# Kernel optimization log

Hardware: AMD Instinct MI355X
Metric: run time of the kernel (lower is better)

Reference implementation:

```python
import jax, jax.numpy as jnp
import numpy as np

EPS_LN1 = 1e-6   # partial(nn.LayerNorm, eps=1e-6)
EPS_OUT = 1e-5   # nn.LayerNorm default inside SS3D out_norm


def _layernorm(x, w, b, eps):
    m = jnp.mean(x, axis=-1, keepdims=True)
    v = jnp.var(x, axis=-1, keepdims=True)
    return (x - m) * jax.lax.rsqrt(v + eps) * w + b


def _selective_scan(dA, dBx):
    # dA, dBx: (B, K, d, L, N); linear recurrence h_t = dA_t * h_{t-1} + dBx_t
    def comb(c1, c2):
        a1, b1 = c1
        a2, b2 = c2
        return a2 * a1, a2 * b1 + b2
    _, hs = jax.lax.associative_scan(comb, (dA, dBx), axis=3)
    return hs  # (B, K, d, L, N)


def setup_inputs() -> dict:
    key = jax.random.key(0)
    ks = jax.random.split(key, 12)
    B, D, H, W, C = 1, 16, 16, 16, 96
    d, N, K, R = 96, 16, 6, 6  # d_inner, d_state, n_scan_dirs, dt_rank
    s = 0.02
    f = lambda k, shp: jax.random.normal(k, shp, dtype=jnp.float32)
    return {
        "x": f(ks[0], (B, D, H, W, C)),
        "ln1_w": jnp.ones((C,), jnp.float32),
        "ln1_b": jnp.zeros((C,), jnp.float32),
        "in_proj_w": f(ks[1], (2 * d, C)) * s,
        "conv_w": f(ks[2], (d, 1, 3, 3, 3)) * s,
        "conv_b": f(ks[3], (d,)) * s,
        "x_proj_w": f(ks[4], (K, R + 2 * N, d)) * s,
        "dt_proj_w": f(ks[5], (K, d, R)) * s,
        "dt_proj_b": f(ks[6], (K, d)) * s,
        "A_log": jnp.log(1.0 + 15.0 * jax.random.uniform(ks[7], (K, d, N), jnp.float32)),
        "D_skip": f(ks[8], (K, d)) * s,
        "out_norm_w": jnp.ones((d,), jnp.float32),
        "out_norm_b": jnp.zeros((d,), jnp.float32),
        "out_proj_w": f(ks[9], (C, d)) * s,
    }


def reference(x, ln1_w, ln1_b, in_proj_w, conv_w, conv_b, x_proj_w,
              dt_proj_w, dt_proj_b, A_log, D_skip, out_norm_w, out_norm_b,
              out_proj_w):
    B, D, H, W, C = x.shape
    L = D * H * W
    K, _, d = x_proj_w.shape
    R = dt_proj_w.shape[2]
    N = A_log.shape[2]

    # pre-norm
    xn = _layernorm(x, ln1_w, ln1_b, EPS_LN1)

    # in_proj -> (x, z)
    xz = jnp.einsum('bdhwc,ec->bdhwe', xn, in_proj_w)  # (B,D,H,W,2d)
    xh, z = jnp.split(xz, 2, axis=-1)

    # depthwise 3x3x3 conv + SiLU, channels-first
    xc = jnp.transpose(xh, (0, 4, 1, 2, 3))  # (B,d,D,H,W)
    xc = jax.lax.conv_general_dilated(
        xc, conv_w, window_strides=(1, 1, 1), padding='SAME',
        dimension_numbers=('NCDHW', 'OIDHW', 'NCDHW'),
        feature_group_count=d)
    xc = jax.nn.silu(xc + conv_b[None, :, None, None, None])

    # K = 6 scan orderings: DHW, HWD, WDH and their reverses
    o0 = xc.reshape(B, d, L)
    o1 = jnp.transpose(xc, (0, 1, 3, 4, 2)).reshape(B, d, L)  # (H,W,D) order
    o2 = jnp.transpose(xc, (0, 1, 4, 2, 3)).reshape(B, d, L)  # (W,D,H) order
    fwd3 = jnp.stack([o0, o1, o2], axis=1)                    # (B,3,d,L)
    xs = jnp.concatenate([fwd3, jnp.flip(fwd3, axis=-1)], axis=1)  # (B,K,d,L)

    # per-direction input-dependent parameters
    x_dbl = jnp.einsum('bkdl,kcd->bkcl', xs, x_proj_w)        # (B,K,R+2N,L)
    dt, Bm, Cm = jnp.split(x_dbl, [R, R + N], axis=2)
    dts = jnp.einsum('bkrl,kdr->bkdl', dt, dt_proj_w) + dt_proj_b[None, :, :, None]
    dts = jax.nn.softplus(dts)                                # delta_softplus

    A = -jnp.exp(A_log)                                       # (K,d,N)
    dA = jnp.exp(dts[..., None] * A[None, :, :, None, :])     # (B,K,d,L,N)
    Bt = jnp.transpose(Bm, (0, 1, 3, 2))                      # (B,K,L,N)
    dBx = (dts * xs)[..., None] * Bt[:, :, None, :, :]        # (B,K,d,L,N)

    hs = _selective_scan(dA, dBx)                             # (B,K,d,L,N)
    Ct = jnp.transpose(Cm, (0, 1, 3, 2))                      # (B,K,L,N)
    ys = jnp.einsum('bkdln,bkln->bkdl', hs, Ct) + D_skip[None, :, :, None] * xs

    # undo reversals and orderings, sum the 6 paths
    yf = ys[:, :3] + jnp.flip(ys[:, 3:], axis=-1)             # (B,3,d,L)
    y0 = yf[:, 0]
    y1 = jnp.transpose(yf[:, 1].reshape(B, d, H, W, D), (0, 1, 4, 2, 3)).reshape(B, d, L)
    y2 = jnp.transpose(yf[:, 2].reshape(B, d, W, D, H), (0, 1, 3, 4, 2)).reshape(B, d, L)
    y = (y0 + y1 + y2).reshape(B, d, D, H, W)
    y = jnp.transpose(y, (0, 2, 3, 4, 1))                     # (B,D,H,W,d)

    # out_norm, gate, out_proj
    y = _layernorm(y, out_norm_w, out_norm_b, EPS_OUT)
    y = y * jax.nn.silu(z)
    out = jnp.einsum('bdhwe,ce->bdhwc', y, out_proj_w)

    # residual (drop_path is identity at eval)
    return x + out
```

## Files before the change

### kernel.cpp

```cpp
#include <hip/hip_runtime.h>
#include <hip/hip_bf16.h>

#define L 4096
#define CDIM 96
#define DDIM 96
#define KDIR 6
#define NST 16
#define RRK 6
#define YH 32
#define NCHUNK 256
#define CHLEN 16

typedef _Float16 half4v __attribute__((ext_vector_type(4)));

__device__ __forceinline__ float sigmoidf_(float x) { return 1.f / (1.f + __expf(-x)); }

__device__ __forceinline__ int sigma_k(int kb, int l) {
    if (kb == 0) return l;
    if (kb == 1) return ((l & 15) << 8) | ((l >> 8) << 4) | ((l >> 4) & 15);
    return (((l >> 4) & 15) << 8) | ((l & 15) << 4) | (l >> 8);
}

__global__ void __launch_bounds__(192) k1_ln_inproj(
        const float* __restrict__ x, const float* __restrict__ ln_w,
        const float* __restrict__ ln_b, const float* __restrict__ Wp,
        _Float16* __restrict__ xhh, _Float16* __restrict__ zsh) {
    int s0 = blockIdx.x * 8;
    int tid = threadIdx.x;
    __shared__ __align__(16) float xt[8][96];
    __shared__ __align__(16) float xn[8][96];
    __shared__ float mss[8], rss[8];
    ((float4*)&xt[0][0])[tid] = ((const float4*)(x + (size_t)s0 * 96))[tid];
    __syncthreads();
    int wave = tid >> 6, lane = tid & 63;
    for (int r = wave; r < 8; r += 3) {
        float v = xt[r][lane] + ((lane < 32) ? xt[r][64 + lane] : 0.f);
#pragma unroll
        for (int off = 1; off < 64; off <<= 1) v += __shfl_xor(v, off);
        float vs = xt[r][lane] * xt[r][lane] + ((lane < 32) ? xt[r][64 + lane] * xt[r][64 + lane] : 0.f);
#pragma unroll
        for (int off = 1; off < 64; off <<= 1) vs += __shfl_xor(vs, off);
        if (lane == 0) {
            float mean = v * (1.f / 96.f);
            float var = vs * (1.f / 96.f) - mean * mean;
            mss[r] = mean; rss[r] = rsqrtf(var + 1e-6f);
        }
    }
    __syncthreads();
    {
        int r = tid / 24, c4 = tid % 24;
        float4 xv = ((float4*)&xt[r][0])[c4];
        float4 wv = ((const float4*)ln_w)[c4];
        float4 bv = ((const float4*)ln_b)[c4];
        float m = mss[r], rs = rss[r];
        float4 o;
        o.x = (xv.x - m) * rs * wv.x + bv.x;
        o.y = (xv.y - m) * rs * wv.y + bv.y;
        o.z = (xv.z - m) * rs * wv.z + bv.z;
        o.w = (xv.w - m) * rs * wv.w + bv.w;
        ((float4*)&xn[r][0])[c4] = o;
    }
    float4 Wr[24];
    const float4* wr = (const float4*)(Wp + (size_t)tid * 96);
#pragma unroll
    for (int c4 = 0; c4 < 24; c4++) Wr[c4] = wr[c4];
    __syncthreads();
#pragma unroll
    for (int s = 0; s < 8; s++) {
        const float4* xr4 = (const float4*)&xn[s][0];
        float a0 = 0.f, a1 = 0.f, a2 = 0.f, a3 = 0.f;
#pragma unroll
        for (int c4 = 0; c4 < 24; c4 += 4) {
            float4 x0 = xr4[c4], x1 = xr4[c4 + 1], x2 = xr4[c4 + 2], x3 = xr4[c4 + 3];
            a0 += Wr[c4].x * x0.x + Wr[c4].y * x0.y + Wr[c4].z * x0.z + Wr[c4].w * x0.w;
            a1 += Wr[c4+1].x * x1.x + Wr[c4+1].y * x1.y + Wr[c4+1].z * x1.z + Wr[c4+1].w * x1.w;
            a2 += Wr[c4+2].x * x2.x + Wr[c4+2].y * x2.y + Wr[c4+2].z * x2.z + Wr[c4+2].w * x2.w;
            a3 += Wr[c4+3].x * x3.x + Wr[c4+3].y * x3.y + Wr[c4+3].z * x3.z + Wr[c4+3].w * x3.w;
        }
        float acc = (a0 + a1) + (a2 + a3);
        if (tid < 96) xhh[(size_t)tid * L + s0 + s] = (_Float16)acc;
        else zsh[(size_t)(s0 + s) * 96 + (tid - 96)] = (_Float16)(acc * sigmoidf_(acc));
    }
}

__global__ void k2_conv(const _Float16* __restrict__ xhh, const float* __restrict__ cw,
                        const float* __restrict__ cb, _Float16* __restrict__ xch,
                        _Float16* __restrict__ xcTh) {
    int idx = blockIdx.x * 256 + threadIdx.x;
    int c = idx >> 12, s = idx & 4095;
    int dz = s >> 8, h = (s >> 4) & 15, w = s & 15;
    const _Float16* xin = xhh + (size_t)c * L;
    const float* wc = cw + c * 27;
    float acc = cb[c];
#pragma unroll
    for (int i = 0; i < 3; i++) {
        int z2 = dz + i - 1; if ((unsigned)z2 > 15u) continue;
#pragma unroll
        for (int j = 0; j < 3; j++) {
            int h2 = h + j - 1; if ((unsigned)h2 > 15u) continue;
#pragma unroll
            for (int kk = 0; kk < 3; kk++) {
                int w2 = w + kk - 1; if ((unsigned)w2 > 15u) continue;
                acc += (float)xin[z2 * 256 + h2 * 16 + w2] * wc[i * 9 + j * 3 + kk];
            }
        }
    }
    float r = acc * sigmoidf_(acc);
    _Float16 hr = (_Float16)r;
    xch[(size_t)c * L + s] = hr;
    xcTh[(size_t)s * 96 + c] = hr;
}

__global__ void k3_xproj(const _Float16* __restrict__ xch, const float* __restrict__ Wx,
                         const float* __restrict__ Wdt, const float* __restrict__ bdt,
                         _Float16* __restrict__ Y2h, _Float16* __restrict__ Zsh) {
    int k = blockIdx.x;
    int tid = threadIdx.x;
    int sbase = blockIdx.y * 256;
    int s = sbase + tid;
    int g = blockIdx.z;
    __shared__ float dts[256][6];
    float acc[14];
#pragma unroll
    for (int i = 0; i < 14; i++) acc[i] = 0.f;
    const float* wdt_rows = Wx + (size_t)k * 38 * DDIM;
    const float* wbc      = Wx + ((size_t)k * 38 + 6 + g * 8) * DDIM;
    for (int dd = 0; dd < 96; dd += 4) {
        float v[4];
#pragma unroll
        for (int j = 0; j < 4; j++) v[j] = (float)xch[(size_t)(dd + j) * L + s];
#pragma unroll
        for (int j = 0; j < 4; j++) {
#pragma unroll
            for (int r = 0; r < 6; r++) acc[r] += wdt_rows[r * DDIM + dd + j] * v[j];
#pragma unroll
            for (int i = 0; i < 8; i++) acc[6 + i] += wbc[i * DDIM + dd + j] * v[j];
        }
    }
    _Float16* yo = Y2h + ((size_t)k * L + s) * YH;
#pragma unroll
    for (int i = 0; i < 8; i++) yo[g * 8 + i] = (_Float16)acc[6 + i];
#pragma unroll
    for (int r = 0; r < 6; r++) dts[tid][r] = acc[r];
    __syncthreads();
    for (int i = 0; i < 24; i++) {
        int idx = i * 256 + tid;
        int dl = idx % 24;
        int sr = idx / 24;
        int d = g * 24 + dl;
        const float* wr = Wdt + ((size_t)k * 96 + d) * 6;
        float a = bdt[k * 96 + d];
#pragma unroll
        for (int r = 0; r < 6; r++) a += wr[r] * dts[sr][r];
        float sp = (a > 15.f) ? a : __logf(1.f + __expf(a));
        Zsh[((size_t)k * L + sbase + sr) * 96 + d] = (_Float16)sp;
    }
}


__global__ void __launch_bounds__(256) ka_scan(
        const _Float16* __restrict__ Zsh, const _Float16* __restrict__ xcTh,
        const _Float16* __restrict__ Y2h, const float* __restrict__ A_log,
        _Float16* __restrict__ Aah, _Float16* __restrict__ Abh) {
    int t = blockIdx.x * 256 + threadIdx.x;
    int nq = t & 3;
    int q = t >> 2;
    int d = q % 96;
    int rest = q / 96;
    int chunk = rest % NCHUNK;
    int k = rest / NCHUNK;
    int kb = (k < 3) ? k : (k - 3);
    bool flip = (k >= 3);
    float An[4];
    {
        float4 al = *(const float4*)(A_log + ((size_t)k * 96 + d) * 16 + nq * 4);
        An[0] = -__expf(al.x); An[1] = -__expf(al.y);
        An[2] = -__expf(al.z); An[3] = -__expf(al.w);
    }
    float a[4] = {1.f, 1.f, 1.f, 1.f};
    float b[4] = {0.f, 0.f, 0.f, 0.f};
    const _Float16* Zk = Zsh + (size_t)k * L * 96;
    const _Float16* Yk = Y2h + (size_t)k * L * YH;
    int l0 = chunk * CHLEN;
    for (int i = 0; i < CHLEN; i += 4) {
        int sI[4]; float dt[4], xv[4]; half4v Bh[4];
#pragma unroll
        for (int j = 0; j < 4; j++) {
            int l = l0 + i + j;
            int lp = flip ? (4095 - l) : l;
            sI[j] = sigma_k(kb, lp);
        }
#pragma unroll
        for (int j = 0; j < 4; j++) {
            dt[j] = (float)Zk[(size_t)sI[j] * 96 + d];
            xv[j] = (float)xcTh[(size_t)sI[j] * 96 + d];
            Bh[j] = *(const half4v*)(Yk + (size_t)sI[j] * YH + nq * 4);
        }
#pragma unroll
        for (int j = 0; j < 4; j++) {
            float dtx = dt[j] * xv[j];
            float e0 = __expf(dt[j] * An[0]);
            float e1 = __expf(dt[j] * An[1]);
            float e2 = __expf(dt[j] * An[2]);
            float e3 = __expf(dt[j] * An[3]);
            b[0] = e0 * b[0] + dtx * (float)Bh[j].x; a[0] *= e0;
            b[1] = e1 * b[1] + dtx * (float)Bh[j].y; a[1] *= e1;
            b[2] = e2 * b[2] + dtx * (float)Bh[j].z; a[2] *= e2;
            b[3] = e3 * b[3] + dtx * (float)Bh[j].w; a[3] *= e3;
        }
    }
    size_t o = (((size_t)k * NCHUNK + chunk) * 96 + d) * 16 + nq * 4;
    half4v ha, hb;
    ha.x = (_Float16)a[0]; ha.y = (_Float16)a[1]; ha.z = (_Float16)a[2]; ha.w = (_Float16)a[3];
    hb.x = (_Float16)b[0]; hb.y = (_Float16)b[1]; hb.z = (_Float16)b[2]; hb.w = (_Float16)b[3];
    *(half4v*)(Aah + o) = ha;
    *(half4v*)(Abh + o) = hb;
}

__global__ void __launch_bounds__(256) kb_combine(
        const _Float16* __restrict__ Aah, const _Float16* __restrict__ Abh,
        _Float16* __restrict__ Pbh) {
    int t = blockIdx.x * 256 + threadIdx.x;
    int n = t & 15;
    int rest = t >> 4;
    int d = rest % 96;
    int k = rest / 96;
    size_t base = ((size_t)k * NCHUNK * 96 + d) * 16 + n;
    const size_t cstride = 96 * 16;
    float rb = 0.f;
    for (int c0 = 0; c0 < NCHUNK; c0 += 16) {
        float av[16], bv[16];
#pragma unroll
        for (int j = 0; j < 16; j++) {
            av[j] = (float)Aah[base + (size_t)(c0 + j) * cstride];
            bv[j] = (float)Abh[base + (size_t)(c0 + j) * cstride];
        }
#pragma unroll
        for (int j = 0; j < 16; j++) {
            Pbh[base + (size_t)(c0 + j) * cstride] = (_Float16)rb;
            rb = av[j] * rb + bv[j];
        }
    }
}

__global__ void __launch_bounds__(256) kc_apply(
        const _Float16* __restrict__ Zsh, const _Float16* __restrict__ xcTh,
        const _Float16* __restrict__ Y2h, const float* __restrict__ A_log,
        const float* __restrict__ D_skip, const _Float16* __restrict__ Pbh,
        _Float16* __restrict__ ysh) {
    int t = blockIdx.x * 256 + threadIdx.x;
    int nq = t & 3;
    int q = t >> 2;
    int d = q % 96;
    int rest = q / 96;
    int chunk = rest % NCHUNK;
    int k = rest / NCHUNK;
    int kb = (k < 3) ? k : (k - 3);
    bool flip = (k >= 3);
    float An[4];
    {
        float4 al = *(const float4*)(A_log + ((size_t)k * 96 + d) * 16 + nq * 4);
        An[0] = -__expf(al.x); An[1] = -__expf(al.y);
        An[2] = -__expf(al.z); An[3] = -__expf(al.w);
    }
    float Dk = D_skip[k * DDIM + d];
    float h[4];
    {
        half4v hp = *(const half4v*)(Pbh + (((size_t)k * NCHUNK + chunk) * 96 + d) * 16 + nq * 4);
        h[0] = (float)hp.x; h[1] = (float)hp.y; h[2] = (float)hp.z; h[3] = (float)hp.w;
    }
    const _Float16* Zk = Zsh + (size_t)k * L * 96;
    const _Float16* Yk = Y2h + (size_t)k * L * YH;
    int l0 = chunk * CHLEN;
    for (int i = 0; i < CHLEN; i += 4) {
        int sI[4]; float dt[4], xv[4]; half4v Bh[4], Ch[4];
#pragma unroll
        for (int j = 0; j < 4; j++) {
            int l = l0 + i + j;
            int lp = flip ? (4095 - l) : l;
            sI[j] = sigma_k(kb, lp);
        }
#pragma unroll
        for (int j = 0; j < 4; j++) {
            dt[j] = (float)Zk[(size_t)sI[j] * 96 + d];
            xv[j] = (float)xcTh[(size_t)sI[j] * 96 + d];
            Bh[j] = *(const half4v*)(Yk + (size_t)sI[j] * YH + nq * 4);
            Ch[j] = *(const half4v*)(Yk + (size_t)sI[j] * YH + 16 + nq * 4);
        }
#pragma unroll
        for (int j = 0; j < 4; j++) {
            float dtx = dt[j] * xv[j];
            float e0 = __expf(dt[j] * An[0]);
            float e1 = __expf(dt[j] * An[1]);
            float e2 = __expf(dt[j] * An[2]);
            float e3 = __expf(dt[j] * An[3]);
            h[0] = e0 * h[0] + dtx * (float)Bh[j].x;
            h[1] = e1 * h[1] + dtx * (float)Bh[j].y;
            h[2] = e2 * h[2] + dtx * (float)Bh[j].z;
            h[3] = e3 * h[3] + dtx * (float)Bh[j].w;
            float p = h[0] * (float)Ch[j].x + h[1] * (float)Ch[j].y
                    + h[2] * (float)Ch[j].z + h[3] * (float)Ch[j].w;
            p += __shfl_xor(p, 1);
            p += __shfl_xor(p, 2);
            if (nq == 0) ysh[((size_t)sI[j] * KDIR + k) * 96 + d] = (_Float16)(p + Dk * xv[j]);
        }
    }
}

__global__ void __launch_bounds__(192) k6_out(
        const _Float16* __restrict__ ysh, const _Float16* __restrict__ zsh,
        const float* __restrict__ onw, const float* __restrict__ onb,
        const float* __restrict__ Wo, const float* __restrict__ x,
        float* __restrict__ out) {
    int s0 = blockIdx.x * 8;
    int tid = threadIdx.x;
    __shared__ __align__(16) float vt[8][96];
    __shared__ __align__(16) float gt[8][96];
    __shared__ float mss[8], rss[8];
#pragma unroll
    for (int j = 0; j < 4; j++) {
        int f = tid + j * 192;
        int sr = f / 96, c = f % 96;
        const _Float16* yr = ysh + ((size_t)(s0 + sr) * KDIR) * 96 + c;
        float v = 0.f;
#pragma unroll
        for (int k = 0; k < KDIR; k++) v += (float)yr[k * 96];
        vt[sr][c] = v;
    }
    __syncthreads();
    int wave = tid >> 6, lane = tid & 63;
    for (int r = wave; r < 8; r += 3) {
        float v = vt[r][lane] + ((lane < 32) ? vt[r][64 + lane] : 0.f);
#pragma unroll
        for (int off = 1; off < 64; off <<= 1) v += __shfl_xor(v, off);
        float vs = vt[r][lane] * vt[r][lane] + ((lane < 32) ? vt[r][64 + lane] * vt[r][64 + lane] : 0.f);
#pragma unroll
        for (int off = 1; off < 64; off <<= 1) vs += __shfl_xor(vs, off);
        if (lane == 0) {
            float mean = v * (1.f / 96.f);
            float var = vs * (1.f / 96.f) - mean * mean;
            mss[r] = mean; rss[r] = rsqrtf(var + 1e-5f);
        }
    }
    __syncthreads();
#pragma unroll
    for (int j = 0; j < 4; j++) {
        int f = tid + j * 192;
        int sr = f / 96, c = f % 96;
        float g = (vt[sr][c] - mss[sr]) * rss[sr] * onw[c] + onb[c];
        gt[sr][c] = g * (float)zsh[(size_t)(s0 + sr) * 96 + c];
    }
    int e = tid % 96, sg = tid / 96;
    float4 Wr[24];
    const float4* wr = (const float4*)(Wo + (size_t)e * 96);
#pragma unroll
    for (int c4 = 0; c4 < 24; c4++) Wr[c4] = wr[c4];
    __syncthreads();
#pragma unroll
    for (int j = 0; j < 4; j++) {
        int s = sg * 4 + j;
        const float4* g4 = (const float4*)&gt[s][0];
        float a0 = 0.f, a1 = 0.f, a2 = 0.f, a3 = 0.f;
#pragma unroll
        for (int c4 = 0; c4 < 24; c4 += 4) {
            float4 x0 = g4[c4], x1 = g4[c4 + 1], x2 = g4[c4 + 2], x3 = g4[c4 + 3];
            a0 += Wr[c4].x * x0.x + Wr[c4].y * x0.y + Wr[c4].z * x0.z + Wr[c4].w * x0.w;
            a1 += Wr[c4+1].x * x1.x + Wr[c4+1].y * x1.y + Wr[c4+1].z * x1.z + Wr[c4+1].w * x1.w;
            a2 += Wr[c4+2].x * x2.x + Wr[c4+2].y * x2.y + Wr[c4+2].z * x2.z + Wr[c4+2].w * x2.w;
            a3 += Wr[c4+3].x * x3.x + Wr[c4+3].y * x3.y + Wr[c4+3].z * x3.z + Wr[c4+3].w * x3.w;
        }
        float acc = (a0 + a1) + (a2 + a3) + x[(size_t)(s0 + s) * 96 + e];
        out[(size_t)(s0 + s) * 96 + e] = acc;
    }
}

extern "C" void kernel_launch(void* const* d_in, const int* in_sizes, int n_in,
                              void* d_out, int out_size, void* d_ws, size_t ws_size,
                              hipStream_t stream) {
    const float* x        = (const float*)d_in[0];
    const float* ln1_w    = (const float*)d_in[1];
    const float* ln1_b    = (const float*)d_in[2];
    const float* in_proj  = (const float*)d_in[3];
    const float* conv_w   = (const float*)d_in[4];
    const float* conv_b   = (const float*)d_in[5];
    const float* x_proj   = (const float*)d_in[6];
    const float* dt_w     = (const float*)d_in[7];
    const float* dt_b     = (const float*)d_in[8];
    const float* A_log    = (const float*)d_in[9];
    const float* D_skip   = (const float*)d_in[10];
    const float* onw      = (const float*)d_in[11];
    const float* onb      = (const float*)d_in[12];
    const float* out_w    = (const float*)d_in[13];
    float* out = (float*)d_out;

    _Float16* xhh  = (_Float16*)d_ws;
    _Float16* zsh  = xhh + (size_t)96 * L;
    _Float16* xch  = zsh + (size_t)96 * L;
    _Float16* xcTh = xch + (size_t)96 * L;
    _Float16* Y2h  = xcTh + (size_t)96 * L;
    _Float16* Zsh  = Y2h + (size_t)KDIR * L * YH;
    _Float16* ysh  = Zsh + (size_t)KDIR * L * 96;
    _Float16* Aah  = ysh + (size_t)L * KDIR * 96;
    _Float16* Abh  = Aah + (size_t)KDIR * NCHUNK * DDIM * NST;
    _Float16* Pbh  = Abh + (size_t)KDIR * NCHUNK * DDIM * NST;

    k1_ln_inproj<<<dim3(L / 8), dim3(192), 0, stream>>>(x, ln1_w, ln1_b, in_proj, xhh, zsh);
    k2_conv<<<dim3(96 * L / 256), dim3(256), 0, stream>>>(xhh, conv_w, conv_b, xch, xcTh);
    k3_xproj<<<dim3(KDIR, 16, 4), dim3(256), 0, stream>>>(xch, x_proj, dt_w, dt_b, Y2h, Zsh);
    ka_scan<<<dim3(KDIR * NCHUNK * DDIM * 4 / 256), dim3(256), 0, stream>>>(Zsh, xcTh, Y2h, A_log, Aah, Abh);
    kb_combine<<<dim3(KDIR * DDIM * NST / 256), dim3(256), 0, stream>>>(Aah, Abh, Pbh);
    kc_apply<<<dim3(KDIR * NCHUNK * DDIM * 4 / 256), dim3(256), 0, stream>>>(Zsh, xcTh, Y2h, A_log, D_skip, Pbh, ysh);
    k6_out<<<dim3(L / 8), dim3(192), 0, stream>>>(ysh, zsh, onw, onb, out_w, x, out);
}
```

Baseline: 179.8 us.

## Parallelize chunk-carry combine with wave-level scan and transpose carry layouts

The chunk-carry combine used to run as a serial loop over 256 chunks per (k,d,n) column with only 9216 threads. It now assigns one 64-lane wave per column: each lane folds 4 chunks, then a shuffle-based Hillis-Steele scan computes the prefix carries. To give that wave contiguous reads, the Aah/Abh/Pbh buffers are stored column-major over chunks, which turns the ka_scan stores and kc_apply loads into strided scalar accesses. The ys buffer is also reordered to put the 6 directions innermost, so k6_out can sum them with three half2 loads while kc_apply's writes become strided.

```diff
diff --git a/kernel.cpp b/kernel.cpp
--- a/kernel.cpp
+++ b/kernel.cpp
@@ -12,6 +12,7 @@
 #define CHLEN 16
 
 typedef _Float16 half4v __attribute__((ext_vector_type(4)));
+typedef _Float16 half2v __attribute__((ext_vector_type(2)));
 
 __device__ __forceinline__ float sigmoidf_(float x) { return 1.f / (1.f + __expf(-x)); }
 
@@ -209,38 +210,41 @@
             b[3] = e3 * b[3] + dtx * (float)Bh[j].w; a[3] *= e3;
         }
     }
-    size_t o = (((size_t)k * NCHUNK + chunk) * 96 + d) * 16 + nq * 4;
-    half4v ha, hb;
-    ha.x = (_Float16)a[0]; ha.y = (_Float16)a[1]; ha.z = (_Float16)a[2]; ha.w = (_Float16)a[3];
-    hb.x = (_Float16)b[0]; hb.y = (_Float16)b[1]; hb.z = (_Float16)b[2]; hb.w = (_Float16)b[3];
-    *(half4v*)(Aah + o) = ha;
-    *(half4v*)(Abh + o) = hb;
+    size_t colbase = ((size_t)(k * 96 + d) * 16 + nq * 4) * NCHUNK + chunk;
+#pragma unroll
+    for (int j = 0; j < 4; j++) {
+        Aah[colbase + (size_t)j * NCHUNK] = (_Float16)a[j];
+        Abh[colbase + (size_t)j * NCHUNK] = (_Float16)b[j];
+    }
 }
 
 __global__ void __launch_bounds__(256) kb_combine(
         const _Float16* __restrict__ Aah, const _Float16* __restrict__ Abh,
         _Float16* __restrict__ Pbh) {
-    int t = blockIdx.x * 256 + threadIdx.x;
-    int n = t & 15;
-    int rest = t >> 4;
-    int d = rest % 96;
-    int k = rest / 96;
-    size_t base = ((size_t)k * NCHUNK * 96 + d) * 16 + n;
-    const size_t cstride = 96 * 16;
-    float rb = 0.f;
-    for (int c0 = 0; c0 < NCHUNK; c0 += 16) {
-        float av[16], bv[16];
-#pragma unroll
-        for (int j = 0; j < 16; j++) {
-            av[j] = (float)Aah[base + (size_t)(c0 + j) * cstride];
-            bv[j] = (float)Abh[base + (size_t)(c0 + j) * cstride];
-        }
-#pragma unroll
-        for (int j = 0; j < 16; j++) {
-            Pbh[base + (size_t)(c0 + j) * cstride] = (_Float16)rb;
-            rb = av[j] * rb + bv[j];
-        }
-    }
+    int w = blockIdx.x * 4 + (threadIdx.x >> 6);
+    int lane = threadIdx.x & 63;
+    size_t colbase = (size_t)w * NCHUNK;
+    half4v ha = *(const half4v*)(Aah + colbase + lane * 4);
+    half4v hb = *(const half4v*)(Abh + colbase + lane * 4);
+    float a0 = (float)ha.x, a1 = (float)ha.y, a2 = (float)ha.z, a3 = (float)ha.w;
+    float b0 = (float)hb.x, b1 = (float)hb.y, b2 = (float)hb.z, b3 = (float)hb.w;
+    float A = a0 * a1 * a2 * a3;
+    float B = ((b0 * a1 + b1) * a2 + b2) * a3 + b3;
+#pragma unroll
+    for (int off = 1; off < 64; off <<= 1) {
+        float Ap = __shfl_up(A, off);
+        float Bp = __shfl_up(B, off);
+        if (lane >= off) { B = A * Bp + B; A = A * Ap; }
+    }
+    float carry = __shfl_up(B, 1);
+    if (lane == 0) carry = 0.f;
+    float P0 = carry;
+    float P1 = a0 * P0 + b0;
+    float P2 = a1 * P1 + b1;
+    float P3 = a2 * P2 + b2;
+    half4v hp;
+    hp.x = (_Float16)P0; hp.y = (_Float16)P1; hp.z = (_Float16)P2; hp.w = (_Float16)P3;
+    *(half4v*)(Pbh + colbase + lane * 4) = hp;
 }
 
 __global__ void __launch_bounds__(256) kc_apply(
@@ -266,8 +270,9 @@
     float Dk = D_skip[k * DDIM + d];
     float h[4];
     {
-        half4v hp = *(const half4v*)(Pbh + (((size_t)k * NCHUNK + chunk) * 96 + d) * 16 + nq * 4);
-        h[0] = (float)hp.x; h[1] = (float)hp.y; h[2] = (float)hp.z; h[3] = (float)hp.w;
+        size_t colbase = ((size_t)(k * 96 + d) * 16 + nq * 4) * NCHUNK + chunk;
+#pragma unroll
+        for (int j = 0; j < 4; j++) h[j] = (float)Pbh[colbase + (size_t)j * NCHUNK];
     }
     const _Float16* Zk = Zsh + (size_t)k * L * 96;
     const _Float16* Yk = Y2h + (size_t)k * L * YH;
@@ -302,7 +307,7 @@
                     + h[2] * (float)Ch[j].z + h[3] * (float)Ch[j].w;
             p += __shfl_xor(p, 1);
             p += __shfl_xor(p, 2);
-            if (nq == 0) ysh[((size_t)sI[j] * KDIR + k) * 96 + d] = (_Float16)(p + Dk * xv[j]);
+            if (nq == 0) ysh[((size_t)sI[j] * 96 + d) * KDIR + k] = (_Float16)(p + Dk * xv[j]);
         }
     }
 }
@@ -321,11 +326,10 @@
     for (int j = 0; j < 4; j++) {
         int f = tid + j * 192;
         int sr = f / 96, c = f % 96;
-        const _Float16* yr = ysh + ((size_t)(s0 + sr) * KDIR) * 96 + c;
-        float v = 0.f;
-#pragma unroll
-        for (int k = 0; k < KDIR; k++) v += (float)yr[k * 96];
-        vt[sr][c] = v;
+        const half2v* yr = (const half2v*)(ysh + ((size_t)(s0 + sr) * 96 + c) * KDIR);
+        half2v y0 = yr[0], y1 = yr[1], y2 = yr[2];
+        vt[sr][c] = (float)y0.x + (float)y0.y + (float)y1.x + (float)y1.y
+                  + (float)y2.x + (float)y2.y;
     }
     __syncthreads();
     int wave = tid >> 6, lane = tid & 63;
@@ -400,15 +404,15 @@
     _Float16* Y2h  = xcTh + (size_t)96 * L;
     _Float16* Zsh  = Y2h + (size_t)KDIR * L * YH;
     _Float16* ysh  = Zsh + (size_t)KDIR * L * 96;
-    _Float16* Aah  = ysh + (size_t)L * KDIR * 96;
-    _Float16* Abh  = Aah + (size_t)KDIR * NCHUNK * DDIM * NST;
-    _Float16* Pbh  = Abh + (size_t)KDIR * NCHUNK * DDIM * NST;
+    _Float16* Aah  = ysh + (size_t)L * 96 * KDIR;
+    _Float16* Abh  = Aah + (size_t)KDIR * DDIM * NST * NCHUNK;
+    _Float16* Pbh  = Abh + (size_t)KDIR * DDIM * NST * NCHUNK;
 
     k1_ln_inproj<<<dim3(L / 8), dim3(192), 0, stream>>>(x, ln1_w, ln1_b, in_proj, xhh, zsh);
     k2_conv<<<dim3(96 * L / 256), dim3(256), 0, stream>>>(xhh, conv_w, conv_b, xch, xcTh);
     k3_xproj<<<dim3(KDIR, 16, 4), dim3(256), 0, stream>>>(xch, x_proj, dt_w, dt_b, Y2h, Zsh);
     ka_scan<<<dim3(KDIR * NCHUNK * DDIM * 4 / 256), dim3(256), 0, stream>>>(Zsh, xcTh, Y2h, A_log, Aah, Abh);
-    kb_combine<<<dim3(KDIR * DDIM * NST / 256), dim3(256), 0, stream>>>(Aah, Abh, Pbh);
+    kb_combine<<<dim3(KDIR * DDIM * NST / 4), dim3(256), 0, stream>>>(Aah, Abh, Pbh);
     kc_apply<<<dim3(KDIR * NCHUNK * DDIM * 4 / 256), dim3(256), 0, stream>>>(Zsh, xcTh, Y2h, A_log, D_skip, Pbh, ysh);
     k6_out<<<dim3(L / 8), dim3(192), 0, stream>>>(ysh, zsh, onw, onb, out_w, x, out);
 }
```

Result: slower. 195.6 us (+8.8%).
